# Kernel optimization log

Measured on AMD Instinct MI355X. Metric: run time of the kernel, lower is better.

## Reference

```python
import jax, jax.numpy as jnp
import numpy as np

N, E, D, H = 50000, 500000, 128, 4
C = D // H
EPS = 1e-5


def _layer_norm(x, g, b):
    mu = jnp.mean(x, axis=-1, keepdims=True)
    var = jnp.mean((x - mu) ** 2, axis=-1, keepdims=True)
    return (x - mu) * jax.lax.rsqrt(var + EPS) * g + b


def setup_inputs() -> dict:
    key = jax.random.key(0)
    ks = jax.random.split(key, 20)
    f = lambda i, shape: jax.random.normal(ks[i], shape, dtype=jnp.float32) * 0.05
    return {
        "x": f(0, (N, D)),
        "edge_index": jax.random.randint(ks[1], (2, E), 0, N),
        "w_gcn": f(2, (D, D)), "b_gcn": f(3, (D,)),
        "wq": f(4, (D, D)), "bq": f(5, (D,)),
        "wk": f(6, (D, D)), "bk": f(7, (D,)),
        "wv": f(8, (D, D)), "bv": f(9, (D,)),
        "w_skip": f(10, (D, D)), "b_skip": f(11, (D,)),
        "w_beta": f(12, (3 * D, 1)),
        "g1": jnp.ones((D,), jnp.float32), "b1": jnp.zeros((D,), jnp.float32),
        "g2": jnp.ones((D,), jnp.float32), "b2": jnp.zeros((D,), jnp.float32),
        "w_rel": f(13, (D, 2 * D)), "w_root": f(14, (2 * D, D)),
        "local_w": jnp.ones((1,), jnp.float32), "global_w": jnp.ones((1,), jnp.float32),
    }


def reference(x, edge_index, w_gcn, b_gcn, wq, bq, wk, bk, wv, bv,
              w_skip, b_skip, w_beta, g1, b1, g2, b2, w_rel, w_root,
              local_w, global_w):
    src, dst = edge_index[0], edge_index[1]

    # ---- GCNConv (add_self_loops=False, symmetric norm) ----
    xw = x @ w_gcn                                   # [N, D]
    deg = jax.ops.segment_sum(jnp.ones((E,), x.dtype), dst, num_segments=N)
    dinv = jnp.where(deg > 0, jax.lax.rsqrt(jnp.maximum(deg, 1.0)), 0.0)
    coef = dinv[src] * dinv[dst]                     # [E]
    local_out = jax.ops.segment_sum(coef[:, None] * xw[src], dst, num_segments=N) + b_gcn

    # ---- TransformerConv (heads=4, concat=True, beta=True) ----
    q = (x @ wq + bq).reshape(N, H, C)
    k = (x @ wk + bk).reshape(N, H, C)
    v = (x @ wv + bv).reshape(N, H, C)
    alpha = jnp.sum(q[dst] * k[src], axis=-1) / jnp.sqrt(jnp.float32(C))  # [E, H]
    m = jax.ops.segment_max(alpha, dst, num_segments=N)
    m = jnp.where(jnp.isfinite(m), m, 0.0)
    a = jnp.exp(alpha - m[dst])
    s = jax.ops.segment_sum(a, dst, num_segments=N)
    attn = a / jnp.maximum(s[dst], 1e-16)            # [E, H] segment softmax over in-edges
    agg = jax.ops.segment_sum(attn[..., None] * v[src], dst, num_segments=N)
    out_g = agg.reshape(N, D)
    x_r = x @ w_skip + b_skip
    beta = jax.nn.sigmoid(jnp.concatenate([out_g, x_r, out_g - x_r], axis=-1) @ w_beta)
    global_out = beta * x_r + (1.0 - beta) * out_g

    # ---- combine + norm + FFN ----
    h = local_w * local_out + global_w * global_out
    h = _layer_norm(h + h, g1, b1)
    out = jax.nn.relu(h @ w_rel) @ w_root
    out = _layer_norm(out + h, g2, b2)
    return out
```

## Files before the change

kernel.cpp:

```cpp
#include <hip/hip_runtime.h>
#include <math.h>

#define D 128
#define EPSV 1e-5f

typedef unsigned short ushort_t;
typedef unsigned char uchar_t;
typedef __attribute__((ext_vector_type(8))) short short8v;
typedef __attribute__((ext_vector_type(4))) float f32x4;
typedef __attribute__((ext_vector_type(2))) float f32x2;
typedef _Float16 half_t;
typedef __attribute__((ext_vector_type(2))) _Float16 h2;

#if __has_builtin(__builtin_amdgcn_cvt_pk_f16_fp8)
#define HAVE_F16P 1
#else
#define HAVE_F16P 0
#endif

__device__ __forceinline__ float bf2f(unsigned u) {
    return __uint_as_float(u << 16);
}
__device__ __forceinline__ ushort_t f2bf(float f) {
    unsigned u = __float_as_uint(f);
    unsigned r = (u + 0x7fffu + ((u >> 16) & 1u)) >> 16;
    return (ushort_t)r;
}
__device__ __forceinline__ float bfp(uint4 v, int i) {
    unsigned w = (&v.x)[i >> 1];
    return bf2f((i & 1) ? (w >> 16) : (w & 0xffffu));
}

__device__ __forceinline__ ushort_t qconv(float f) {
#if HAVE_F16P
    half_t h = (half_t)f;
    return __builtin_bit_cast(ushort_t, h);
#else
    return f2bf(f);
#endif
}

#define UNPACK8_FP8(u, o) { \
    f32x2 _a = __builtin_amdgcn_cvt_pk_f32_fp8((int)(u).x, false); \
    f32x2 _b = __builtin_amdgcn_cvt_pk_f32_fp8((int)(u).x, true);  \
    f32x2 _c = __builtin_amdgcn_cvt_pk_f32_fp8((int)(u).y, false); \
    f32x2 _d = __builtin_amdgcn_cvt_pk_f32_fp8((int)(u).y, true);  \
    o[0] = _a.x; o[1] = _a.y; o[2] = _b.x; o[3] = _b.y;            \
    o[4] = _c.x; o[5] = _c.y; o[6] = _d.x; o[7] = _d.y; }

__device__ __forceinline__ unsigned bf4_to_fp8x4(unsigned w0, unsigned w1) {
    int u = __builtin_amdgcn_cvt_pk_fp8_f32(bf2f(w0 & 0xffffu), bf2f(w0 >> 16), 0, false);
    u = __builtin_amdgcn_cvt_pk_fp8_f32(bf2f(w1 & 0xffffu), bf2f(w1 >> 16), u, true);
    return (unsigned)u;
}

__global__ __launch_bounds__(256)
void proj_gemm(const float* __restrict__ x,
               const ushort_t* __restrict__ Bt,
               const float* __restrict__ bias,
               const float* __restrict__ dinv,
               uchar_t* __restrict__ pack, ushort_t* __restrict__ qb,
               ushort_t* __restrict__ xrb, int M)
{
    __shared__ ushort_t Cs[128 * 136];
    const int tid = threadIdx.x, lane = tid & 63, wid = tid >> 6;
    const int wr = wid >> 1, wc = wid & 1;
    const int R0 = blockIdx.x * 128;
    const int cbeg = blockIdx.y ? 3 : 0;
    const int cend = blockIdx.y ? 5 : 3;

    short8v av[4][4];
    #pragma unroll
    for (int r = 0; r < 4; ++r) {
        int gr = R0 + wr * 64 + r * 16 + (lane & 15);
        if (gr >= M) gr = M - 1;
        const float* xrow = x + (size_t)gr * 128 + (lane >> 4) * 8;
        #pragma unroll
        for (int ks = 0; ks < 4; ++ks) {
            float4 lo = *reinterpret_cast<const float4*>(xrow + ks * 32);
            float4 hi = *reinterpret_cast<const float4*>(xrow + ks * 32 + 4);
            short8v a;
            a[0] = (short)f2bf(lo.x); a[1] = (short)f2bf(lo.y);
            a[2] = (short)f2bf(lo.z); a[3] = (short)f2bf(lo.w);
            a[4] = (short)f2bf(hi.x); a[5] = (short)f2bf(hi.y);
            a[6] = (short)f2bf(hi.z); a[7] = (short)f2bf(hi.w);
            av[r][ks] = a;
        }
    }

    for (int ct = cbeg; ct < cend; ++ct) {
        f32x4 acc[4][4] = {};
        #pragma unroll
        for (int ks = 0; ks < 4; ++ks) {
            short8v bv[4];
            #pragma unroll
            for (int c = 0; c < 4; ++c) {
                int col = ct * 128 + wc * 64 + c * 16 + (lane & 15);
                bv[c] = *reinterpret_cast<const short8v*>(
                    &Bt[(size_t)col * 128 + ks * 32 + (lane >> 4) * 8]);
            }
            #pragma unroll
            for (int r = 0; r < 4; ++r)
                #pragma unroll
                for (int c = 0; c < 4; ++c)
                    acc[r][c] = __builtin_amdgcn_mfma_f32_16x16x32_bf16(av[r][ks], bv[c], acc[r][c], 0, 0, 0);
        }
        __syncthreads();
        #pragma unroll
        for (int r = 0; r < 4; ++r) {
            int rowb = wr * 64 + r * 16 + (lane >> 4) * 4;
            #pragma unroll
            for (int i = 0; i < 4; ++i) {
                float sc = 1.f;
                if (ct == 0) {
                    int grow = R0 + rowb + i;
                    if (grow >= M) grow = M - 1;
                    sc = dinv[grow];
                }
                #pragma unroll
                for (int c = 0; c < 4; ++c) {
                    int col = wc * 64 + c * 16 + (lane & 15);
                    float val = acc[r][c][i] + bias[ct * 128 + col];
                    if (ct == 0) val *= sc;
                    Cs[(rowb + i) * 136 + col] = (ct == 1) ? qconv(val) : f2bf(val);
                }
            }
        }
        __syncthreads();
        if (ct == 1 || ct == 4) {
            #pragma unroll
            for (int it = 0; it < 8; ++it) {
                int linear = tid + it * 256;
                int row = linear >> 4, ch = linear & 15;
                int gr = R0 + row;
                if (gr < M) {
                    uint4 v = *reinterpret_cast<const uint4*>(&Cs[row * 136 + ch * 8]);
                    ushort_t* dst = (ct == 1) ? (qb + (size_t)gr * 128)
                                              : (xrb + (size_t)gr * 128);
                    *reinterpret_cast<uint4*>(dst + ch * 8) = v;
                }
            }
        } else {
            const int byteoff = (ct == 0) ? 256 : (ct == 2) ? 0 : 128;
            #pragma unroll
            for (int it = 0; it < 4; ++it) {
                int linear = tid + it * 256;
                int row = linear >> 3, ch = linear & 7;
                int gr = R0 + row;
                if (gr < M) {
                    uint4 lo = *reinterpret_cast<const uint4*>(&Cs[row * 136 + ch * 16]);
                    uint4 hi = *reinterpret_cast<const uint4*>(&Cs[row * 136 + ch * 16 + 8]);
                    uint4 o;
                    o.x = bf4_to_fp8x4(lo.x, lo.y);
                    o.y = bf4_to_fp8x4(lo.z, lo.w);
                    o.z = bf4_to_fp8x4(hi.x, hi.y);
                    o.w = bf4_to_fp8x4(hi.z, hi.w);
                    *reinterpret_cast<uint4*>(pack + (size_t)gr * 384 + byteoff + ch * 16) = o;
                }
            }
        }
    }
}

__device__ __forceinline__ int swz(int ch, int row) {
    return (ch & 24) | ((ch ^ row) & 7);
}

__global__ __launch_bounds__(256)
void ffn_fused(const ushort_t* __restrict__ hlnb,
               const ushort_t* __restrict__ wt_rel,
               const ushort_t* __restrict__ wt_root,
               const float* __restrict__ g2, const float* __restrict__ b2,
               float* __restrict__ outf, int M)
{
    __shared__ float smem[128 * 130];
    ushort_t* Hs = (ushort_t*)smem;
    const int tid = threadIdx.x, lane = tid & 63, wid = tid >> 6;
    const int wr = wid >> 1, wc = wid & 1;
    const int R0 = blockIdx.x * 128;

    short8v av[4][4];
    #pragma unroll
    for (int r = 0; r < 4; ++r) {
        int gr = R0 + wr * 64 + r * 16 + (lane & 15);
        if (gr >= M) gr = M - 1;
        #pragma unroll
        for (int ks = 0; ks < 4; ++ks)
            av[r][ks] = *reinterpret_cast<const short8v*>(
                &hlnb[(size_t)gr * 128 + ks * 32 + (lane >> 4) * 8]);
    }
    for (int ct = 0; ct < 2; ++ct) {
        f32x4 acc[4][4] = {};
        #pragma unroll
        for (int ks = 0; ks < 4; ++ks) {
            short8v bv[4];
            #pragma unroll
            for (int c = 0; c < 4; ++c) {
                int col = ct * 128 + wc * 64 + c * 16 + (lane & 15);
                bv[c] = *reinterpret_cast<const short8v*>(
                    &wt_rel[(size_t)col * 128 + ks * 32 + (lane >> 4) * 8]);
            }
            #pragma unroll
            for (int r = 0; r < 4; ++r)
                #pragma unroll
                for (int c = 0; c < 4; ++c)
                    acc[r][c] = __builtin_amdgcn_mfma_f32_16x16x32_bf16(av[r][ks], bv[c], acc[r][c], 0, 0, 0);
        }
        #pragma unroll
        for (int r = 0; r < 4; ++r) {
            int rowb = wr * 64 + r * 16 + (lane >> 4) * 4;
            #pragma unroll
            for (int i = 0; i < 4; ++i)
                #pragma unroll
                for (int c = 0; c < 4; ++c) {
                    int row = rowb + i;
                    int col = ct * 128 + wc * 64 + c * 16 + (lane & 15);
                    int ch = col >> 3, el = col & 7;
                    Hs[row * 256 + swz(ch, row) * 8 + el] = f2bf(fmaxf(acc[r][c][i], 0.f));
                }
        }
    }
    __syncthreads();

    f32x4 acc2[4][4] = {};
    #pragma unroll
    for (int ks = 0; ks < 8; ++ks) {
        short8v a2[4], bv[4];
        #pragma unroll
        for (int r = 0; r < 4; ++r) {
            int row = wr * 64 + r * 16 + (lane & 15);
            int ch = ks * 4 + (lane >> 4);
            a2[r] = *reinterpret_cast<const short8v*>(&Hs[row * 256 + swz(ch, row) * 8]);
        }
        #pragma unroll
        for (int c = 0; c < 4; ++c) {
            int col = wc * 64 + c * 16 + (lane & 15);
            bv[c] = *reinterpret_cast<const short8v*>(
                &wt_root[(size_t)col * 256 + ks * 32 + (lane >> 4) * 8]);
        }
        #pragma unroll
        for (int r = 0; r < 4; ++r)
            #pragma unroll
            for (int c = 0; c < 4; ++c)
                acc2[r][c] = __builtin_amdgcn_mfma_f32_16x16x32_bf16(a2[r], bv[c], acc2[r][c], 0, 0, 0);
    }
    __syncthreads();

    float* Cs = smem;
    #pragma unroll
    for (int r = 0; r < 4; ++r) {
        int rowb = wr * 64 + r * 16 + (lane >> 4) * 4;
        #pragma unroll
        for (int i = 0; i < 4; ++i)
            #pragma unroll
            for (int c = 0; c < 4; ++c)
                Cs[(rowb + i) * 130 + wc * 64 + c * 16 + (lane & 15)] = acc2[r][c][i];
    }
    __syncthreads();

    const float ga = g2[lane * 2], gb = g2[lane * 2 + 1];
    const float ba = b2[lane * 2], bb2 = b2[lane * 2 + 1];
    for (int rr = 0; rr < 32; ++rr) {
        int row = wid * 32 + rr;
        int gr = R0 + row;
        if (gr >= M) break;
        unsigned hu = *reinterpret_cast<const unsigned*>(&hlnb[(size_t)gr * 128 + lane * 2]);
        float t0 = Cs[row * 130 + lane * 2]     + bf2f(hu & 0xffffu);
        float t1 = Cs[row * 130 + lane * 2 + 1] + bf2f(hu >> 16);
        float ssum = t0 + t1;
        #pragma unroll
        for (int off = 1; off <= 32; off <<= 1) ssum += __shfl_xor(ssum, off);
        float mu = ssum * (1.f / 128.f);
        float dv0 = t0 - mu, dv1 = t1 - mu;
        float vsum = dv0 * dv0 + dv1 * dv1;
        #pragma unroll
        for (int off = 1; off <= 32; off <<= 1) vsum += __shfl_xor(vsum, off);
        float rs = rsqrtf(vsum * (1.f / 128.f) + EPSV);
        float2 o = make_float2(dv0 * rs * ga + ba, dv1 * rs * gb + bb2);
        *reinterpret_cast<float2*>(&outf[(size_t)gr * 128 + lane * 2]) = o;
    }
}

__global__ __launch_bounds__(256)
void scan1_packw_kernel(const int* __restrict__ deg, int* __restrict__ row_start,
                        int* __restrict__ bsum, int n, int SB,
                        const float* __restrict__ wg, const float* __restrict__ wq,
                        const float* __restrict__ wk, const float* __restrict__ wv,
                        const float* __restrict__ wsk,
                        const float* __restrict__ bq, const float* __restrict__ bk,
                        const float* __restrict__ bv, const float* __restrict__ bsk,
                        const float* __restrict__ wrel, const float* __restrict__ wroot,
                        ushort_t* __restrict__ wt_all, ushort_t* __restrict__ wt_rel,
                        ushort_t* __restrict__ wt_root, float* __restrict__ bias_all)
{
    __shared__ int ws[4];
    if ((int)blockIdx.x < SB) {
        const int t = threadIdx.x, lane = t & 63, wid = t >> 6;
        const int base = blockIdx.x * 1024 + t * 4;
        int v0 = 0, v1 = 0, v2 = 0, v3 = 0;
        if (base + 3 < n) {
            int4 q = *reinterpret_cast<const int4*>(&deg[base]);
            v0 = q.x; v1 = q.y; v2 = q.z; v3 = q.w;
        } else {
            if (base < n)     v0 = deg[base];
            if (base + 1 < n) v1 = deg[base + 1];
            if (base + 2 < n) v2 = deg[base + 2];
            if (base + 3 < n) v3 = deg[base + 3];
        }
        int tot = v0 + v1 + v2 + v3;
        int inc = tot;
        #pragma unroll
        for (int off = 1; off < 64; off <<= 1) {
            int y = __shfl_up(inc, off);
            if (lane >= off) inc += y;
        }
        if (lane == 63) ws[wid] = inc;
        __syncthreads();
        int woff = 0;
        for (int w = 0; w < wid; ++w) woff += ws[w];
        int excl = woff + inc - tot;
        if (base < n)     row_start[base]     = excl;
        if (base + 1 < n) row_start[base + 1] = excl + v0;
        if (base + 2 < n) row_start[base + 2] = excl + v0 + v1;
        if (base + 3 < n) row_start[base + 3] = excl + v0 + v1 + v2;
        if (t == 0) bsum[blockIdx.x] = ws[0] + ws[1] + ws[2] + ws[3];
    } else {
        int i = (blockIdx.x - SB) * 256 + threadIdx.x;
        if (i < 640 * 128) {
            int c = i >> 7, k = i & 127;
            const float* srcs[5] = {wg, wq, wk, wv, wsk};
            wt_all[i] = f2bf(srcs[c >> 7][k * 128 + (c & 127)]);
        } else if (i < 640 * 128 + 256 * 128) {
            int j = i - 640 * 128;
            int c = j >> 7, k = j & 127;
            wt_rel[j] = f2bf(wrel[k * 256 + c]);
        } else if (i < 640 * 128 + 256 * 128 + 128 * 256) {
            int j = i - (640 * 128 + 256 * 128);
            int c = j >> 8, k = j & 255;
            wt_root[j] = f2bf(wroot[k * 128 + c]);
        } else if (i < 640 * 128 + 256 * 128 + 128 * 256 + 640) {
            int c = i - (640 * 128 + 256 * 128 + 128 * 256);
            float b = 0.f;
            if (c >= 128) {
                const float* bs[4] = {bq, bk, bv, bsk};
                b = bs[(c - 128) >> 7][c & 127];
            }
            bias_all[c] = b;
        }
    }
}

__global__ void deg_count_kernel(const int* __restrict__ dst, int* __restrict__ deg, int E)
{
    int e = blockIdx.x * blockDim.x + threadIdx.x;
    if (e < E) atomicAdd(&deg[dst[e]], 1);
}

__global__ __launch_bounds__(256)
void scan3_kernel(const int* __restrict__ deg, const int* __restrict__ bsum,
                  int* __restrict__ row_start, int* __restrict__ cursor,
                  float* __restrict__ dinv, int n, int E)
{
    __shared__ int boff_s;
    const int K = blockIdx.x >> 2;
    if (threadIdx.x == 0) {
        int s = 0;
        for (int j = 0; j < K; ++j) s += bsum[j];
        boff_s = s;
    }
    __syncthreads();
    int i = blockIdx.x * 256 + threadIdx.x;
    if (i < n) {
        int rs = row_start[i] + boff_s;
        row_start[i] = rs;
        cursor[i] = rs;
        int d = deg[i];
        dinv[i] = (d > 0) ? rsqrtf((float)d) : 0.f;
    }
    if (i == 0) row_start[n] = E;
}

__global__ void fill_kernel(const int* __restrict__ src, const int* __restrict__ dst,
                            int* __restrict__ cursor, int* __restrict__ csr_src, int E)
{
    int e = blockIdx.x * blockDim.x + threadIdx.x;
    if (e < E) {
        int d = dst[e];
        int pos = atomicAdd(&cursor[d], 1);
        csr_src[pos] = src[e];
    }
}

__global__ __launch_bounds__(256)
void edge_fused_kernel(const uchar_t* __restrict__ pack,
                       const ushort_t* __restrict__ qbf,
                       const ushort_t* __restrict__ xrbf,
                       const int* __restrict__ row_start,
                       const int* __restrict__ csr_src,
                       const float* __restrict__ dinv,
                       const float* __restrict__ b_gcn,
                       const float* __restrict__ w_beta,
                       const float* __restrict__ g1, const float* __restrict__ b1,
                       const float* __restrict__ local_w, const float* __restrict__ global_w,
                       ushort_t* __restrict__ hln_bf, int n)
{
    const int wid = threadIdx.x >> 6, lane = threadIdx.x & 63;
    const int node = blockIdx.x * 4 + wid;
    if (node >= n) return;
    const int slot = lane >> 4, li = lane & 15;
    const int d8 = li * 8;

    const int e0 = row_start[node], e1 = row_start[node + 1];
    const float dn = dinv[node];
    const float scale = 0.17677669529663687f;

    float s = 0.f;
    float va[8], ga[8];

#if HAVE_F16P
    uint4 qu = *reinterpret_cast<const uint4*>(&qbf[(size_t)node * 128 + d8]);
    h2 qh[4] = { __builtin_bit_cast(h2, qu.x), __builtin_bit_cast(h2, qu.y),
                 __builtin_bit_cast(h2, qu.z), __builtin_bit_cast(h2, qu.w) };
    h2 va2[4] = {}, ga2[4] = {};
    for (int j = e0; j < e1; j += 4) {
        const int je = j + slot;
        const bool act = je < e1;
        const int sidx = act ? csr_src[je] : n;
        const uchar_t* prow = pack + (size_t)sidx * 384;
        uint2 ku = *reinterpret_cast<const uint2*>(prow + d8);
        uint2 vu = *reinterpret_cast<const uint2*>(prow + 128 + d8);
        uint2 xu = *reinterpret_cast<const uint2*>(prow + 256 + d8);
        h2 k0 = __builtin_amdgcn_cvt_pk_f16_fp8((short)(ku.x & 0xffffu));
        h2 k1 = __builtin_amdgcn_cvt_pk_f16_fp8((short)(ku.x >> 16));
        h2 k2 = __builtin_amdgcn_cvt_pk_f16_fp8((short)(ku.y & 0xffffu));
        h2 k3 = __builtin_amdgcn_cvt_pk_f16_fp8((short)(ku.y >> 16));
        h2 pd = k0 * qh[0] + k1 * qh[1] + k2 * qh[2] + k3 * qh[3];
        float p = (float)pd[0] + (float)pd[1];
        p += __shfl_xor(p, 1);
        p += __shfl_xor(p, 2);
        float wgt = act ? __expf(p * scale) : 0.f;
        s += wgt;
        half_t wh = (half_t)wgt;
        h2 w2 = { wh, wh };
        h2 v0 = __builtin_amdgcn_cvt_pk_f16_fp8((short)(vu.x & 0xffffu));
        h2 v1 = __builtin_amdgcn_cvt_pk_f16_fp8((short)(vu.x >> 16));
        h2 v2 = __builtin_amdgcn_cvt_pk_f16_fp8((short)(vu.y & 0xffffu));
        h2 v3 = __builtin_amdgcn_cvt_pk_f16_fp8((short)(vu.y >> 16));
        va2[0] += w2 * v0; va2[1] += w2 * v1; va2[2] += w2 * v2; va2[3] += w2 * v3;
        h2 x0 = __builtin_amdgcn_cvt_pk_f16_fp8((short)(xu.x & 0xffffu));
        h2 x1 = __builtin_amdgcn_cvt_pk_f16_fp8((short)(xu.x >> 16));
        h2 x2 = __builtin_amdgcn_cvt_pk_f16_fp8((short)(xu.y & 0xffffu));
        h2 x3 = __builtin_amdgcn_cvt_pk_f16_fp8((short)(xu.y >> 16));
        ga2[0] += x0; ga2[1] += x1; ga2[2] += x2; ga2[3] += x3;
    }
    #pragma unroll
    for (int i = 0; i < 4; ++i) {
        va[2 * i] = (float)va2[i][0]; va[2 * i + 1] = (float)va2[i][1];
        ga[2 * i] = (float)ga2[i][0]; ga[2 * i + 1] = (float)ga2[i][1];
    }
#else
    uint4 qu = *reinterpret_cast<const uint4*>(&qbf[(size_t)node * 128 + d8]);
    float q[8];
    #pragma unroll
    for (int i = 0; i < 8; ++i) q[i] = bfp(qu, i);
    #pragma unroll
    for (int i = 0; i < 8; ++i) { va[i] = 0.f; ga[i] = 0.f; }
    for (int j = e0; j < e1; j += 4) {
        const int je = j + slot;
        const bool act = je < e1;
        const int sidx = act ? csr_src[je] : n;
        const uchar_t* prow = pack + (size_t)sidx * 384;
        uint2 ku = *reinterpret_cast<const uint2*>(prow + d8);
        uint2 vu = *reinterpret_cast<const uint2*>(prow + 128 + d8);
        uint2 xu = *reinterpret_cast<const uint2*>(prow + 256 + d8);
        float kf[8], vf[8], xf[8];
        UNPACK8_FP8(ku, kf);
        UNPACK8_FP8(vu, vf);
        UNPACK8_FP8(xu, xf);
        float p = 0.f;
        #pragma unroll
        for (int i = 0; i < 8; ++i) p = fmaf(q[i], kf[i], p);
        p += __shfl_xor(p, 1);
        p += __shfl_xor(p, 2);
        float wgt = act ? __expf(p * scale) : 0.f;
        s += wgt;
        #pragma unroll
        for (int i = 0; i < 8; ++i) {
            va[i] = fmaf(wgt, vf[i], va[i]);
            ga[i] += xf[i];
        }
    }
#endif

    #pragma unroll
    for (int off = 16; off <= 32; off <<= 1) {
        s += __shfl_xor(s, off);
        #pragma unroll
        for (int i = 0; i < 8; ++i) {
            va[i] += __shfl_xor(va[i], off);
            ga[i] += __shfl_xor(ga[i], off);
        }
    }
    const float denom = fmaxf(s, 1e-16f);

    uint4 xru = *reinterpret_cast<const uint4*>(&xrbf[(size_t)node * 128 + d8]);
    float t[8];
    float part = 0.f;
    #pragma unroll
    for (int i = 0; i < 8; ++i) {
        float og = va[i] / denom;
        float xr = bfp(xru, i);
        float lo = dn * ga[i] + b_gcn[d8 + i];
        part += og * w_beta[d8 + i] + xr * w_beta[128 + d8 + i]
              + (og - xr) * w_beta[256 + d8 + i];
        t[i] = lo;
        va[i] = og; ga[i] = xr;
    }
    #pragma unroll
    for (int off = 1; off <= 32; off <<= 1) part += __shfl_xor(part, off);
    const float beta = 1.f / (1.f + __expf(-part * 0.25f));

    const float lw = local_w[0], gw = global_w[0];
    float ssum = 0.f;
    #pragma unroll
    for (int i = 0; i < 8; ++i) {
        float go = beta * ga[i] + (1.f - beta) * va[i];
        t[i] = 2.f * (lw * t[i] + gw * go);
        ssum += t[i];
    }
    #pragma unroll
    for (int off = 1; off <= 32; off <<= 1) ssum += __shfl_xor(ssum, off);
    const float mu = ssum * (1.f / 512.f);
    float vsum = 0.f;
    #pragma unroll
    for (int i = 0; i < 8; ++i) { float d = t[i] - mu; vsum += d * d; }
    #pragma unroll
    for (int off = 1; off <= 32; off <<= 1) vsum += __shfl_xor(vsum, off);
    const float rs = rsqrtf(vsum * (1.f / 512.f) + EPSV);

    if (slot == 0) {
        uint4 o;
        #pragma unroll
        for (int i = 0; i < 4; ++i) {
            float o0 = (t[2*i]   - mu) * rs * g1[d8 + 2*i]   + b1[d8 + 2*i];
            float o1 = (t[2*i+1] - mu) * rs * g1[d8 + 2*i+1] + b1[d8 + 2*i+1];
            (&o.x)[i] = (unsigned)f2bf(o0) | ((unsigned)f2bf(o1) << 16);
        }
        *reinterpret_cast<uint4*>(&hln_bf[(size_t)node * 128 + d8]) = o;
    }
}

extern "C" void kernel_launch(void* const* d_in, const int* in_sizes, int n_in,
                              void* d_out, int out_size, void* d_ws, size_t ws_size,
                              hipStream_t stream)
{
    const float* x      = (const float*)d_in[0];
    const int*   ei     = (const int*)d_in[1];
    const float* w_gcn  = (const float*)d_in[2];
    const float* b_gcn  = (const float*)d_in[3];
    const float* wq     = (const float*)d_in[4];
    const float* bq     = (const float*)d_in[5];
    const float* wk     = (const float*)d_in[6];
    const float* bk     = (const float*)d_in[7];
    const float* wv     = (const float*)d_in[8];
    const float* bv     = (const float*)d_in[9];
    const float* w_skip = (const float*)d_in[10];
    const float* b_skip = (const float*)d_in[11];
    const float* w_beta = (const float*)d_in[12];
    const float* g1     = (const float*)d_in[13];
    const float* b1     = (const float*)d_in[14];
    const float* g2     = (const float*)d_in[15];
    const float* b2     = (const float*)d_in[16];
    const float* w_rel  = (const float*)d_in[17];
    const float* w_root = (const float*)d_in[18];
    const float* lw     = (const float*)d_in[19];
    const float* gw     = (const float*)d_in[20];

    const int N = in_sizes[0] / D;
    const int E = in_sizes[1] / 2;
    const int* src = ei;
    const int* dst = ei + E;

    char* wsb = (char*)d_ws;
    size_t off = 0;
    auto alloc = [&](size_t bytes) -> void* {
        void* p = wsb + off;
        off += (bytes + 255) & ~(size_t)255;
        return p;
    };
    uchar_t*  pack_kvx = (uchar_t*)alloc((size_t)(N + 1) * 384);
    ushort_t* qb_bf    = (ushort_t*)alloc((size_t)N * 128 * 2);
    ushort_t* xr_bf    = (ushort_t*)alloc((size_t)N * 128 * 2);
    ushort_t* hln_bf   = (ushort_t*)alloc((size_t)N * 128 * 2);
    ushort_t* wt_all   = (ushort_t*)alloc(640 * 128 * 2);
    ushort_t* wt_rel   = (ushort_t*)alloc(256 * 128 * 2);
    ushort_t* wt_root  = (ushort_t*)alloc(128 * 256 * 2);
    float*    bias_all = (float*)alloc(640 * 4);
    int*      deg      = (int*)alloc((size_t)N * 4);
    int*      row_start= (int*)alloc((size_t)(N + 1) * 4);
    int*      cursor   = (int*)alloc((size_t)N * 4);
    int*      csr_src  = (int*)alloc((size_t)E * 4);
    float*    dinv     = (float*)alloc((size_t)N * 4);
    int*      bsum     = (int*)alloc(((size_t)(N + 1023) / 1024) * 4);

    float* out = (float*)d_out;
    const int SB = (N + 1023) / 1024;

    hipMemsetAsync(deg, 0, (size_t)N * sizeof(int), stream);
    hipMemsetAsync(pack_kvx + (size_t)N * 384, 0, 384, stream);
    deg_count_kernel<<<dim3((E + 255) / 256), dim3(256), 0, stream>>>(dst, deg, E);
    scan1_packw_kernel<<<dim3(SB + 579), dim3(256), 0, stream>>>(
        deg, row_start, bsum, N, SB,
        w_gcn, wq, wk, wv, w_skip, bq, bk, bv, b_skip, w_rel, w_root,
        wt_all, wt_rel, wt_root, bias_all);
    scan3_kernel<<<dim3((N + 255) / 256), dim3(256), 0, stream>>>(
        deg, bsum, row_start, cursor, dinv, N, E);
    fill_kernel<<<dim3((E + 255) / 256), dim3(256), 0, stream>>>(src, dst, cursor, csr_src, E);

    const int MB = (N + 127) / 128;
    proj_gemm<<<dim3(MB, 2), dim3(256), 0, stream>>>(
        x, wt_all, bias_all, dinv, pack_kvx, qb_bf, xr_bf, N);

    edge_fused_kernel<<<dim3((N + 3) / 4), dim3(256), 0, stream>>>(
        pack_kvx, qb_bf, xr_bf, row_start, csr_src, dinv, b_gcn, w_beta,
        g1, b1, lw, gw, hln_bf, N);

    ffn_fused<<<dim3(MB), dim3(256), 0, stream>>>(
        hln_bf, wt_rel, wt_root, g2, b2, out, N);
}
```

Baseline: 219.2 us.

## Pre-convert x to bf16 and split projection GEMM into one block per column tile

Adds a separate kernel that converts x from fp32 to bf16 once. The projection GEMM now launches 5 column tiles in grid y instead of looping over 2-3 tiles per block, which raises the block count and drops the per-block loop and extra barriers. The scan3 prefix offset is now summed by a 64-lane wave reduction instead of a single serial thread. The cost is an extra kernel launch and a bf16 copy of x written to and read back from memory, and each x tile is loaded 5 times instead of twice.

```diff
diff --git a/kernel.cpp b/kernel.cpp
--- a/kernel.cpp
+++ b/kernel.cpp
@@ -54,8 +54,23 @@
     return (unsigned)u;
 }
 
+__global__ void cvt_bf16_kernel(const float* __restrict__ in, ushort_t* __restrict__ out, int n8)
+{
+    int i = blockIdx.x * blockDim.x + threadIdx.x;
+    if (i < n8) {
+        float4 a = reinterpret_cast<const float4*>(in)[i * 2];
+        float4 b = reinterpret_cast<const float4*>(in)[i * 2 + 1];
+        uint4 o;
+        o.x = (unsigned)f2bf(a.x) | ((unsigned)f2bf(a.y) << 16);
+        o.y = (unsigned)f2bf(a.z) | ((unsigned)f2bf(a.w) << 16);
+        o.z = (unsigned)f2bf(b.x) | ((unsigned)f2bf(b.y) << 16);
+        o.w = (unsigned)f2bf(b.z) | ((unsigned)f2bf(b.w) << 16);
+        reinterpret_cast<uint4*>(out)[i] = o;
+    }
+}
+
 __global__ __launch_bounds__(256)
-void proj_gemm(const float* __restrict__ x,
+void proj_gemm(const ushort_t* __restrict__ xbf,
                const ushort_t* __restrict__ Bt,
                const float* __restrict__ bias,
                const float* __restrict__ dinv,
@@ -66,97 +81,87 @@
     const int tid = threadIdx.x, lane = tid & 63, wid = tid >> 6;
     const int wr = wid >> 1, wc = wid & 1;
     const int R0 = blockIdx.x * 128;
-    const int cbeg = blockIdx.y ? 3 : 0;
-    const int cend = blockIdx.y ? 5 : 3;
+    const int ct = blockIdx.y;
 
     short8v av[4][4];
     #pragma unroll
     for (int r = 0; r < 4; ++r) {
         int gr = R0 + wr * 64 + r * 16 + (lane & 15);
         if (gr >= M) gr = M - 1;
-        const float* xrow = x + (size_t)gr * 128 + (lane >> 4) * 8;
-        #pragma unroll
-        for (int ks = 0; ks < 4; ++ks) {
-            float4 lo = *reinterpret_cast<const float4*>(xrow + ks * 32);
-            float4 hi = *reinterpret_cast<const float4*>(xrow + ks * 32 + 4);
-            short8v a;
-            a[0] = (short)f2bf(lo.x); a[1] = (short)f2bf(lo.y);
-            a[2] = (short)f2bf(lo.z); a[3] = (short)f2bf(lo.w);
-            a[4] = (short)f2bf(hi.x); a[5] = (short)f2bf(hi.y);
-            a[6] = (short)f2bf(hi.z); a[7] = (short)f2bf(hi.w);
-            av[r][ks] = a;
-        }
-    }
-
-    for (int ct = cbeg; ct < cend; ++ct) {
-        f32x4 acc[4][4] = {};
-        #pragma unroll
-        for (int ks = 0; ks < 4; ++ks) {
-            short8v bv[4];
+        #pragma unroll
+        for (int ks = 0; ks < 4; ++ks)
+            av[r][ks] = *reinterpret_cast<const short8v*>(
+                &xbf[(size_t)gr * 128 + ks * 32 + (lane >> 4) * 8]);
+    }
+
+    f32x4 acc[4][4] = {};
+    #pragma unroll
+    for (int ks = 0; ks < 4; ++ks) {
+        short8v bv[4];
+        #pragma unroll
+        for (int c = 0; c < 4; ++c) {
+            int col = ct * 128 + wc * 64 + c * 16 + (lane & 15);
+            bv[c] = *reinterpret_cast<const short8v*>(
+                &Bt[(size_t)col * 128 + ks * 32 + (lane >> 4) * 8]);
+        }
+        #pragma unroll
+        for (int r = 0; r < 4; ++r)
+            #pragma unroll
+            for (int c = 0; c < 4; ++c)
+                acc[r][c] = __builtin_amdgcn_mfma_f32_16x16x32_bf16(av[r][ks], bv[c], acc[r][c], 0, 0, 0);
+    }
+
+    #pragma unroll
+    for (int r = 0; r < 4; ++r) {
+        int rowb = wr * 64 + r * 16 + (lane >> 4) * 4;
+        #pragma unroll
+        for (int i = 0; i < 4; ++i) {
+            float sc = 1.f;
+            if (ct == 0) {
+                int grow = R0 + rowb + i;
+                if (grow >= M) grow = M - 1;
+                sc = dinv[grow];
+            }
             #pragma unroll
             for (int c = 0; c < 4; ++c) {
-                int col = ct * 128 + wc * 64 + c * 16 + (lane & 15);
-                bv[c] = *reinterpret_cast<const short8v*>(
-                    &Bt[(size_t)col * 128 + ks * 32 + (lane >> 4) * 8]);
+                int col = wc * 64 + c * 16 + (lane & 15);
+                float val = acc[r][c][i] + bias[ct * 128 + col];
+                if (ct == 0) val *= sc;
+                Cs[(rowb + i) * 136 + col] = (ct == 1) ? qconv(val) : f2bf(val);
             }
-            #pragma unroll
-            for (int r = 0; r < 4; ++r)
-                #pragma unroll
-                for (int c = 0; c < 4; ++c)
-                    acc[r][c] = __builtin_amdgcn_mfma_f32_16x16x32_bf16(av[r][ks], bv[c], acc[r][c], 0, 0, 0);
-        }
-        __syncthreads();
-        #pragma unroll
-        for (int r = 0; r < 4; ++r) {
-            int rowb = wr * 64 + r * 16 + (lane >> 4) * 4;
-            #pragma unroll
-            for (int i = 0; i < 4; ++i) {
-                float sc = 1.f;
-                if (ct == 0) {
-                    int grow = R0 + rowb + i;
-                    if (grow >= M) grow = M - 1;
-                    sc = dinv[grow];
-                }
-                #pragma unroll
-                for (int c = 0; c < 4; ++c) {
-                    int col = wc * 64 + c * 16 + (lane & 15);
-                    float val = acc[r][c][i] + bias[ct * 128 + col];
-                    if (ct == 0) val *= sc;
-                    Cs[(rowb + i) * 136 + col] = (ct == 1) ? qconv(val) : f2bf(val);
-                }
+        }
+    }
+    __syncthreads();
+
+    if (ct == 1 || ct == 4) {
+        #pragma unroll
+        for (int it = 0; it < 8; ++it) {
+            int linear = tid + it * 256;
+            int row = linear >> 4, ch = linear & 15;
+            int gr = R0 + row;
+            if (gr < M) {
+                uint4 v = *reinterpret_cast<const uint4*>(&Cs[row * 136 + ch * 8]);
+                ushort_t* dst = (ct == 1) ? (qb + (size_t)gr * 128)
+                                          : (xrb + (size_t)gr * 128);
+                *reinterpret_cast<uint4*>(dst + ch * 8) = v;
             }
         }
-        __syncthreads();
-        if (ct == 1 || ct == 4) {
-            #pragma unroll
-            for (int it = 0; it < 8; ++it) {
-                int linear = tid + it * 256;
-                int row = linear >> 4, ch = linear & 15;
-                int gr = R0 + row;
-                if (gr < M) {
-                    uint4 v = *reinterpret_cast<const uint4*>(&Cs[row * 136 + ch * 8]);
-                    ushort_t* dst = (ct == 1) ? (qb + (size_t)gr * 128)
-                                              : (xrb + (size_t)gr * 128);
-                    *reinterpret_cast<uint4*>(dst + ch * 8) = v;
-                }
-            }
-        } else {
-            const int byteoff = (ct == 0) ? 256 : (ct == 2) ? 0 : 128;
-            #pragma unroll
-            for (int it = 0; it < 4; ++it) {
-                int linear = tid + it * 256;
-                int row = linear >> 3, ch = linear & 7;
-                int gr = R0 + row;
-                if (gr < M) {
-                    uint4 lo = *reinterpret_cast<const uint4*>(&Cs[row * 136 + ch * 16]);
-                    uint4 hi = *reinterpret_cast<const uint4*>(&Cs[row * 136 + ch * 16 + 8]);
-                    uint4 o;
-                    o.x = bf4_to_fp8x4(lo.x, lo.y);
-                    o.y = bf4_to_fp8x4(lo.z, lo.w);
-                    o.z = bf4_to_fp8x4(hi.x, hi.y);
-                    o.w = bf4_to_fp8x4(hi.z, hi.w);
-                    *reinterpret_cast<uint4*>(pack + (size_t)gr * 384 + byteoff + ch * 16) = o;
-                }
+    } else {
+        const int byteoff = (ct == 0) ? 256 : (ct == 2) ? 0 : 128;
+        #pragma unroll
+        for (int it = 0; it < 4; ++it) {
+            int linear = tid + it * 256;
+            int row = linear >> 3, ch = linear & 7;
+            int gr = R0 + row;
+            if (gr < M) {
+                uint4 lo = *reinterpret_cast<const uint4*>(&Cs[row * 136 + ch * 16]);
+                uint4 hi = *reinterpret_cast<const uint4*>(&Cs[row * 136 + ch * 16 + 8]);
+                uint4 o;
+                o.x = bf4_to_fp8x4(lo.x, lo.y);
+                o.y = bf4_to_fp8x4(lo.z, lo.w);
+                o.z = bf4_to_fp8x4(hi.x, hi.y);
+                o.w = bf4_to_fp8x4(hi.z, hi.w);
+                *reinterpret_cast<uint4*>(pack + (size_t)gr * 384 + byteoff + ch * 16) = o;
             }
         }
     }
@@ -363,13 +368,16 @@
 {
     __shared__ int boff_s;
     const int K = blockIdx.x >> 2;
-    if (threadIdx.x == 0) {
-        int s = 0;
-        for (int j = 0; j < K; ++j) s += bsum[j];
-        boff_s = s;
+    const int t = threadIdx.x;
+    if (t < 64) {
+        int v = 0;
+        for (int j = t; j < K; j += 64) v += bsum[j];
+        #pragma unroll
+        for (int off = 1; off <= 32; off <<= 1) v += __shfl_xor(v, off);
+        if (t == 0) boff_s = v;
     }
     __syncthreads();
-    int i = blockIdx.x * 256 + threadIdx.x;
+    int i = blockIdx.x * 256 + t;
     if (i < n) {
         int rs = row_start[i] + boff_s;
         row_start[i] = rs;
@@ -589,6 +597,7 @@
         return p;
     };
     uchar_t*  pack_kvx = (uchar_t*)alloc((size_t)(N + 1) * 384);
+    ushort_t* xbf      = (ushort_t*)alloc((size_t)N * 128 * 2);
     ushort_t* qb_bf    = (ushort_t*)alloc((size_t)N * 128 * 2);
     ushort_t* xr_bf    = (ushort_t*)alloc((size_t)N * 128 * 2);
     ushort_t* hln_bf   = (ushort_t*)alloc((size_t)N * 128 * 2);
@@ -608,6 +617,7 @@
 
     hipMemsetAsync(deg, 0, (size_t)N * sizeof(int), stream);
     hipMemsetAsync(pack_kvx + (size_t)N * 384, 0, 384, stream);
+    cvt_bf16_kernel<<<dim3((N * 16 + 255) / 256), dim3(256), 0, stream>>>(x, xbf, N * 16);
     deg_count_kernel<<<dim3((E + 255) / 256), dim3(256), 0, stream>>>(dst, deg, E);
     scan1_packw_kernel<<<dim3(SB + 579), dim3(256), 0, stream>>>(
         deg, row_start, bsum, N, SB,
@@ -618,8 +628,8 @@
     fill_kernel<<<dim3((E + 255) / 256), dim3(256), 0, stream>>>(src, dst, cursor, csr_src, E);
 
     const int MB = (N + 127) / 128;
-    proj_gemm<<<dim3(MB, 2), dim3(256), 0, stream>>>(
-        x, wt_all, bias_all, dinv, pack_kvx, qb_bf, xr_bf, N);
+    proj_gemm<<<dim3(MB, 5), dim3(256), 0, stream>>>(
+        xbf, wt_all, bias_all, dinv, pack_kvx, qb_bf, xr_bf, N);
 
     edge_fused_kernel<<<dim3((N + 3) / 4), dim3(256), 0, stream>>>(
         pack_kvx, qb_bf, xr_bf, row_start, csr_src, dinv, b_gcn, w_beta,
```

After: 210.0 us. 1.04x faster.
